# Kernel optimization log

Hardware: AMD Instinct MI355X
Metric: run time of the kernel (lower is better)

The kernel has to match this reference:

```python
import jax, jax.numpy as jnp
import numpy as np

B, Q, L, D = 4, 600, 2048, 256
H, HD, DFF, KD = 8, 32, 2048, 32  # heads, head_dim, ffn dim, gasa kernel dim
SCALE = HD ** -0.5


def setup_inputs() -> dict:
    key = jax.random.key(0)
    ks = jax.random.split(key, 24)
    w = lambda k, shape, s=0.02: (jax.random.normal(k, shape, jnp.float32) * s)
    inp = {
        "queries": jax.random.normal(ks[0], (B, Q, D), jnp.float32),
        "memory": jax.random.normal(ks[1], (B, L, D), jnp.float32),
        "memory_pos": jax.random.normal(ks[2], (B, L, 3), jnp.float32),
        "query_pos": jax.random.normal(ks[3], (B, Q, 3), jnp.float32),
        # self-attention (nn.MultiheadAttention packed in_proj)
        "sa_in_w": w(ks[4], (3 * D, D)), "sa_in_b": jnp.zeros((3 * D,), jnp.float32),
        "sa_out_w": w(ks[5], (D, D)), "sa_out_b": jnp.zeros((D,), jnp.float32),
        "norm1_g": jnp.ones((D,), jnp.float32), "norm1_b": jnp.zeros((D,), jnp.float32),
        # cross-attention projections
        "q_w": w(ks[6], (D, D)), "q_b": jnp.zeros((D,), jnp.float32),
        "k_w": w(ks[7], (D, D)), "k_b": jnp.zeros((D,), jnp.float32),
        "v_w": w(ks[8], (D, D)), "v_b": jnp.zeros((D,), jnp.float32),
        "o_w": w(ks[9], (D, D)), "o_b": jnp.zeros((D,), jnp.float32),
        "norm2_g": jnp.ones((D,), jnp.float32), "norm2_b": jnp.zeros((D,), jnp.float32),
        # GASA geometric-bias kernel: beta, MLP 1->KD->1
        "beta": jnp.asarray(1.0, jnp.float32),
        "dk_w1": w(ks[10], (KD, 1), 0.1), "dk_b1": jnp.zeros((KD,), jnp.float32),
        "dk_w2": w(ks[11], (1, KD), 0.1), "dk_b2": jnp.full((1,), -1.0, jnp.float32),
        # FFN
        "ffn_w1": w(ks[12], (DFF, D)), "ffn_b1": jnp.zeros((DFF,), jnp.float32),
        "ffn_w2": w(ks[13], (D, DFF)), "ffn_b2": jnp.zeros((D,), jnp.float32),
        "norm3_g": jnp.ones((D,), jnp.float32), "norm3_b": jnp.zeros((D,), jnp.float32),
    }
    return inp


def _ln(x, g, b, eps=1e-5):
    m = jnp.mean(x, -1, keepdims=True)
    v = jnp.mean((x - m) ** 2, -1, keepdims=True)
    return (x - m) * jax.lax.rsqrt(v + eps) * g + b


def _heads(x, wt, b):  # x:[B,N,D] -> [B,H,N,HD]
    y = x @ wt.T + b
    return y.reshape(x.shape[0], x.shape[1], H, HD).transpose(0, 2, 1, 3)


def reference(queries, memory, memory_pos, query_pos,
              sa_in_w, sa_in_b, sa_out_w, sa_out_b, norm1_g, norm1_b,
              q_w, q_b, k_w, k_b, v_w, v_b, o_w, o_b, norm2_g, norm2_b,
              beta, dk_w1, dk_b1, dk_w2, dk_b2,
              ffn_w1, ffn_b1, ffn_w2, ffn_b2, norm3_g, norm3_b):
    # ---- self-attention (post-norm, no query_pe) ----
    wq, wk, wv = jnp.split(sa_in_w, 3, axis=0)
    bq, bk, bv = jnp.split(sa_in_b, 3)
    qh = _heads(queries, wq, bq)
    kh = _heads(queries, wk, bk)
    vh = _heads(queries, wv, bv)
    a = jax.nn.softmax(jnp.einsum('bhqd,bhkd->bhqk', qh, kh) * SCALE, axis=-1)
    sa = jnp.einsum('bhqk,bhkd->bhqd', a, vh).transpose(0, 2, 1, 3).reshape(B, Q, D)
    sa = sa @ sa_out_w.T + sa_out_b
    x = _ln(queries + sa, norm1_g, norm1_b)

    # ---- GASA cross-attention ----
    Qh = _heads(x, q_w, q_b)          # [B,H,Q,HD]
    Kh = _heads(memory, k_w, k_b)     # [B,H,L,HD]
    Vh = _heads(memory, v_w, v_b)     # [B,H,L,HD]
    # cdist + learned kernel MLP, clamp to [-10, 0] (suppress-only)
    d2 = jnp.sum((query_pos[:, :, None, :] - memory_pos[:, None, :, :]) ** 2, -1)
    dist = jnp.sqrt(jnp.maximum(d2, 0.0))                     # [B,Q,L]
    hid = jax.nn.relu(dist[..., None] * dk_w1[:, 0] + dk_b1)  # [B,Q,L,KD]
    bias = (hid @ dk_w2[0]) + dk_b2[0]                        # [B,Q,L]
    bias = jnp.clip(bias, -10.0, 0.0)
    scores = jnp.einsum('bhqd,bhkd->bhqk', Qh, Kh) * SCALE + beta * bias[:, None]
    attn = jax.nn.softmax(scores, axis=-1)
    ca = jnp.einsum('bhqk,bhkd->bhqd', attn, Vh).transpose(0, 2, 1, 3).reshape(B, Q, D)
    ca = ca @ o_w.T + o_b
    x = _ln(x + ca, norm2_g, norm2_b)

    # ---- FFN (post-norm) ----
    f = jax.nn.relu(x @ ffn_w1.T + ffn_b1) @ ffn_w2.T + ffn_b2
    return _ln(x + f, norm3_g, norm3_b)
```

## Files before the change

### kernel.cpp

```cpp
#include <hip/hip_runtime.h>
#include <hip/hip_bf16.h>

typedef __hip_bfloat16 bf16;
typedef __attribute__((ext_vector_type(8))) short  short8;
typedef __attribute__((ext_vector_type(4))) short  short4v;
typedef __attribute__((ext_vector_type(4))) float  f32x4;

#define B_ 4
#define Q_ 600
#define L_ 2048
#define D_ 256
#define H_ 8
#define HD_ 32
#define DFF_ 2048
#define KD_ 32
#define SCALE_ 0.17677669529663687f
#define L2E_   1.4426950408889634f
#define SL2E_  (SCALE_ * L2E_)

template<int MODE>
__device__ __forceinline__ float ldx(const void* p, size_t i, bool f32)
{
    if (MODE == 0) return __bfloat162float(((const bf16*)p)[i]);
    if (MODE == 1) return ((const float*)p)[i];
    return f32 ? ((const float*)p)[i] : __bfloat162float(((const bf16*)p)[i]);
}
__device__ __forceinline__ short8 ld8_f32(const float* p)
{
    const float4 a = *(const float4*)p;
    const float4 b = *(const float4*)(p + 4);
    union { short8 s; bf16 h[8]; } u;
    u.h[0] = __float2bfloat16(a.x); u.h[1] = __float2bfloat16(a.y);
    u.h[2] = __float2bfloat16(a.z); u.h[3] = __float2bfloat16(a.w);
    u.h[4] = __float2bfloat16(b.x); u.h[5] = __float2bfloat16(b.y);
    u.h[6] = __float2bfloat16(b.z); u.h[7] = __float2bfloat16(b.w);
    return u.s;
}
template<int MODE>
__device__ __forceinline__ short8 ld8x(const void* p, size_t i, bool f32)
{
    if (MODE == 0) return *(const short8*)((const bf16*)p + i);
    if (MODE == 1) return ld8_f32((const float*)p + i);
    return f32 ? ld8_f32((const float*)p + i) : *(const short8*)((const bf16*)p + i);
}

__global__ __launch_bounds__(256)
void detect_kernel(const unsigned short* __restrict__ q, int* __restrict__ flag)
{
    __shared__ float red[4];
    const int tid = threadIdx.x;
    unsigned short u = q[tid];
    float f = __uint_as_float(((unsigned)(u & 0x7FFF)) << 16);
    if (f != f) f = 1e30f;
    #pragma unroll
    for (int o = 32; o > 0; o >>= 1) f = fmaxf(f, __shfl_xor(f, o));
    if ((tid & 63) == 0) red[tid >> 6] = f;
    __syncthreads();
    if (tid == 0) {
        float m = fmaxf(fmaxf(red[0], red[1]), fmaxf(red[2], red[3]));
        *flag = (m > 100.f) ? 1 : 0;
    }
}

template<int AM>
__device__ __forceinline__ void gemm_core(const void* __restrict__ A,
    const void* __restrict__ W, int M, int K, int kbeg, int kend,
    int bm, int bn, bool f32, bf16* As, bf16* Bs, f32x4 (&acc)[2][2])
{
    const int tid = threadIdx.x;
    const int w = tid >> 6, lane = tid & 63;
    const int quad = lane >> 4, l16 = lane & 15;
    const int wm = (w & 1) << 5, wn = (w >> 1) << 5;
    const int srow = tid >> 2, scol = (tid & 3) << 3;
    const int gma = (bm + srow < M) ? bm + srow : M - 1;

    short8 pa = ld8x<AM>(A, (size_t)gma * K + kbeg + scol, f32);
    short8 pb = ld8x<2>(W, (size_t)(bn + srow) * K + kbeg + scol, f32);

    for (int k0 = kbeg; k0 < kend; k0 += 32) {
        *(short8*)&As[srow * 40 + scol] = pa;
        *(short8*)&Bs[srow * 40 + scol] = pb;
        __syncthreads();
        if (k0 + 32 < kend) {
            pa = ld8x<AM>(A, (size_t)gma * K + k0 + 32 + scol, f32);
            pb = ld8x<2>(W, (size_t)(bn + srow) * K + k0 + 32 + scol, f32);
        }
        short8 af[2], bfr[2];
        #pragma unroll
        for (int t = 0; t < 2; t++) {
            af[t]  = *(const short8*)&As[(wm + t * 16 + l16) * 40 + quad * 8];
            bfr[t] = *(const short8*)&Bs[(wn + t * 16 + l16) * 40 + quad * 8];
        }
        #pragma unroll
        for (int mt = 0; mt < 2; mt++)
            #pragma unroll
            for (int nt = 0; nt < 2; nt++)
                acc[mt][nt] = __builtin_amdgcn_mfma_f32_16x16x32_bf16(
                    af[mt], bfr[nt], acc[mt][nt], 0, 0, 0);
        __syncthreads();
    }
}

template<int AM, int RM, int CM, bool RELU, int SPLIT>
__global__ __launch_bounds__(256)
void gemm_mfma(const void* __restrict__ A, const void* __restrict__ W,
               const void* __restrict__ bias, const void* __restrict__ R,
               void* __restrict__ C, int M, int N, int K,
               const int* __restrict__ flagp)
{
    const bool f32 = (*flagp != 0);
    __shared__ alignas(16) bf16 As[64 * 40];
    __shared__ alignas(16) bf16 Bs[64 * 40];
    const int bm = blockIdx.y << 6, bn = blockIdx.x << 6;
    const int KS = K / SPLIT, z = (SPLIT > 1) ? blockIdx.z : 0;

    f32x4 acc[2][2] = {{{0.f,0.f,0.f,0.f},{0.f,0.f,0.f,0.f}},
                       {{0.f,0.f,0.f,0.f},{0.f,0.f,0.f,0.f}}};
    gemm_core<AM>(A, W, M, K, z * KS, z * KS + KS, bm, bn, f32, As, Bs, acc);

    const int tid = threadIdx.x;
    const int w = tid >> 6, lane = tid & 63;
    const int quad = lane >> 4, l16 = lane & 15;
    const int wm = (w & 1) << 5, wn = (w >> 1) << 5;

    #pragma unroll
    for (int mt = 0; mt < 2; mt++) {
        #pragma unroll
        for (int r = 0; r < 4; r++) {
            const int row = bm + wm + mt * 16 + quad * 4 + r;
            if (row >= M) continue;
            #pragma unroll
            for (int nt = 0; nt < 2; nt++) {
                const int col = bn + wn + nt * 16 + l16;
                if (SPLIT > 1) {
                    ((float*)C)[((size_t)z * M + row) * N + col] = acc[mt][nt][r];
                } else {
                    float v = acc[mt][nt][r] + ldx<2>(bias, col, f32);
                    if (RM >= 0) v += ldx<RM < 0 ? 0 : RM>(R, (size_t)row * N + col, f32);
                    if (RELU) v = fmaxf(v, 0.f);
                    if (CM == 0) ((bf16*)C)[(size_t)row * N + col] = __float2bfloat16(v);
                    else         ((float*)C)[(size_t)row * N + col] = v;
                }
            }
        }
    }
}

__global__ __launch_bounds__(256)
void kv_proj(const void* __restrict__ A,
             const void* __restrict__ kw, const void* __restrict__ kb,
             const void* __restrict__ vw, const void* __restrict__ vb,
             bf16* __restrict__ kf, bf16* __restrict__ vf,
             int M, int K, const int* __restrict__ flagp)
{
    const bool f32 = (*flagp != 0);
    __shared__ alignas(16) bf16 As[64 * 40];
    __shared__ alignas(16) bf16 Bs[64 * 40];
    const int sel = blockIdx.x >> 2;
    const void* W  = sel ? vw : kw;
    const void* bs = sel ? vb : kb;
    bf16* C        = sel ? vf : kf;
    const int bn = (blockIdx.x & 3) << 6;
    const int bm = blockIdx.y << 6;

    f32x4 acc[2][2] = {{{0.f,0.f,0.f,0.f},{0.f,0.f,0.f,0.f}},
                       {{0.f,0.f,0.f,0.f},{0.f,0.f,0.f,0.f}}};
    gemm_core<2>(A, W, M, K, 0, K, bm, bn, f32, As, Bs, acc);

    const int tid = threadIdx.x;
    const int w = tid >> 6, lane = tid & 63;
    const int quad = lane >> 4, l16 = lane & 15;
    const int wm = (w & 1) << 5, wn = (w >> 1) << 5;
    #pragma unroll
    for (int mt = 0; mt < 2; mt++)
        #pragma unroll
        for (int r = 0; r < 4; r++) {
            const int row = bm + wm + mt * 16 + quad * 4 + r;
            if (row >= M) continue;
            #pragma unroll
            for (int nt = 0; nt < 2; nt++) {
                const int col = bn + wn + nt * 16 + l16;
                C[(size_t)row * 256 + col] =
                    __float2bfloat16(acc[mt][nt][r] + ldx<2>(bs, col, f32));
            }
        }
}

template<int RM, int OM, int S>
__global__ __launch_bounds__(64)
void red_ln(const float* __restrict__ P, const void* __restrict__ bias,
            const void* __restrict__ R, const void* __restrict__ gg,
            const void* __restrict__ bb, void* __restrict__ Y,
            int M, const int* __restrict__ flagp)
{
    const bool f32 = (*flagp != 0);
    const int row = blockIdx.x, lane = threadIdx.x;
    const int d0 = lane * 4;
    float v[4];
    {
        float4 a = *(const float4*)(P + ((size_t)0 * M + row) * D_ + d0);
        v[0] = a.x; v[1] = a.y; v[2] = a.z; v[3] = a.w;
    }
    #pragma unroll
    for (int s = 1; s < S; s++) {
        float4 a = *(const float4*)(P + ((size_t)s * M + row) * D_ + d0);
        v[0] += a.x; v[1] += a.y; v[2] += a.z; v[3] += a.w;
    }
    #pragma unroll
    for (int j = 0; j < 4; j++)
        v[j] += ldx<2>(bias, d0 + j, f32) + ldx<RM>(R, (size_t)row * D_ + d0 + j, f32);

    float s1 = v[0] + v[1] + v[2] + v[3];
    float s2 = v[0]*v[0] + v[1]*v[1] + v[2]*v[2] + v[3]*v[3];
    #pragma unroll
    for (int o = 32; o > 0; o >>= 1) {
        s1 += __shfl_xor(s1, o);
        s2 += __shfl_xor(s2, o);
    }
    const float mean = s1 * (1.f / D_);
    const float var = s2 * (1.f / D_) - mean * mean;
    const float rinv = rsqrtf(var + 1e-5f);
    float o[4];
    #pragma unroll
    for (int j = 0; j < 4; j++)
        o[j] = (v[j] - mean) * rinv * ldx<2>(gg, d0 + j, f32) + ldx<2>(bb, d0 + j, f32);
    const size_t i = (size_t)row * D_ + d0;
    if (OM == 1 || (OM == 2 && f32)) {
        float4 t{o[0], o[1], o[2], o[3]};
        *(float4*)((float*)Y + i) = t;
    } else {
        bf16* y = (bf16*)Y + i;
        y[0] = __float2bfloat16(o[0]); y[1] = __float2bfloat16(o[1]);
        y[2] = __float2bfloat16(o[2]); y[3] = __float2bfloat16(o[3]);
    }
}

template<bool HASBIAS, int NSEG>
__global__ __launch_bounds__(256)
void flash_attn(const bf16* __restrict__ Qm, int qs,
                const bf16* __restrict__ Km, int ks,
                const bf16* __restrict__ Vm, int vs,
                const bf16* __restrict__ biasT,
                bf16* __restrict__ pO, float* __restrict__ pml,
                int NQ, int LK)
{
    __shared__ alignas(16) bf16 Ksh[64 * 40];
    __shared__ alignas(16) bf16 Vt[48 * 72];
    __shared__ alignas(16) bf16 Psh[64 * 72];
    __shared__ alignas(16) bf16 Bsh[HASBIAS ? 64 * 72 : 8];

    const int tid = threadIdx.x;
    const int w = tid >> 6, lane = tid & 63;
    const int quad = lane >> 4, l16 = lane & 15;

    const int id = blockIdx.x;
    const int g  = ((id >> 6) << 3) + (id & 7);
    const int h  = (id >> 3) & 7;
    const int qt = g % 10;
    const int zz = g / 10;
    const int b = zz & 3, seg = zz >> 2;
    const int q0 = qt * 64;
    const int segLen = LK / NSEG;
    const int lbeg = seg * segLen, lend = lbeg + segLen;

    for (int i = tid; i < 16 * 72; i += 256) {
        int rr = 32 + i / 72, cc = i % 72;
        Vt[rr * 72 + cc] = __float2bfloat16(rr == 32 ? 1.f : 0.f);
    }

    int qrow = q0 + w * 16 + l16; if (qrow > NQ - 1) qrow = NQ - 1;
    const short8 aq = *(const short8*)(Qm + (size_t)(b * NQ + qrow) * qs + h * HD_ + quad * 8);

    f32x4 O0 = {0.f,0.f,0.f,0.f}, O1 = {0.f,0.f,0.f,0.f}, O2 = {0.f,0.f,0.f,0.f};

    const int srow = tid >> 2, sc4 = tid & 3;
    const int nch = (segLen + 63) >> 6;

    for (int ch = 0; ch < nch; ch++) {
        const int l0 = lbeg + (ch << 6);
        {
            int lg = l0 + srow; if (lg > LK - 1) lg = LK - 1;
            short8 k8 = *(const short8*)(Km + (size_t)(b * LK + lg) * ks + h * HD_ + sc4 * 8);
            *(short8*)&Ksh[srow * 40 + sc4 * 8] = k8;
            short8 v8 = *(const short8*)(Vm + (size_t)(b * LK + lg) * vs + h * HD_ + sc4 * 8);
            const int swc = srow ^ (sc4 * 16);
            #pragma unroll
            for (int j = 0; j < 8; j++)
                Vt[(sc4 * 8 + j) * 72 + swc] = ((const bf16*)&v8)[j];
            if (HASBIAS) {
                #pragma unroll
                for (int rep = 0; rep < 2; rep++) {
                    int chid = tid + rep * 256;
                    int ll = chid >> 3, qc = chid & 7;
                    int qread = q0 + qc * 8;
                    if (qread > NQ - 8) qread = NQ - 8;
                    *(short8*)&Bsh[ll * 72 + qc * 8] =
                        *(const short8*)(biasT + ((size_t)(b * LK) + l0 + ll) * Q_ + qread);
                }
            }
        }
        __syncthreads();

        f32x4 sv[4];
        #pragma unroll
        for (int jt = 0; jt < 4; jt++) {
            short8 kb = *(const short8*)&Ksh[(jt * 16 + l16) * 40 + quad * 8];
            sv[jt] = __builtin_amdgcn_mfma_f32_16x16x32_bf16(aq, kb, (f32x4){0.f,0.f,0.f,0.f}, 0, 0, 0);
        }
        if (l0 + 64 <= lend) {
            #pragma unroll
            for (int jt = 0; jt < 4; jt++) {
                if (HASBIAS) {
                    short4v bb = *(const short4v*)&Bsh[(jt * 16 + l16) * 72 + w * 16 + quad * 4];
                    #pragma unroll
                    for (int r = 0; r < 4; r++)
                        Psh[(w * 16 + quad * 4 + r) * 72 + jt * 16 + l16] =
                            __float2bfloat16(exp2f(sv[jt][r] * SL2E_ +
                                __bfloat162float(((const bf16*)&bb)[r])));
                } else {
                    #pragma unroll
                    for (int r = 0; r < 4; r++)
                        Psh[(w * 16 + quad * 4 + r) * 72 + jt * 16 + l16] =
                            __float2bfloat16(exp2f(sv[jt][r] * SL2E_));
                }
            }
        } else {
            #pragma unroll
            for (int jt = 0; jt < 4; jt++) {
                const bool valid = (l0 + jt * 16 + l16) < lend;
                #pragma unroll
                for (int r = 0; r < 4; r++)
                    Psh[(w * 16 + quad * 4 + r) * 72 + jt * 16 + l16] =
                        __float2bfloat16(valid ? exp2f(sv[jt][r] * SL2E_) : 0.f);
            }
        }
        __syncthreads();
        const int sw0 = 16 * (l16 >> 3);
        const int sw1 = 16 * (2 + (l16 >> 3));
        #pragma unroll
        for (int kt = 0; kt < 2; kt++) {
            short8 ap  = *(const short8*)&Psh[(w * 16 + l16) * 72 + kt * 32 + quad * 8];
            short8 bv0 = *(const short8*)&Vt[(l16) * 72 + ((kt * 32 + quad * 8) ^ sw0)];
            short8 bv1 = *(const short8*)&Vt[(16 + l16) * 72 + ((kt * 32 + quad * 8) ^ sw1)];
            short8 bon = *(const short8*)&Vt[(32 + l16) * 72 + kt * 32 + quad * 8];
            O0 = __builtin_amdgcn_mfma_f32_16x16x32_bf16(ap, bv0, O0, 0, 0, 0);
            O1 = __builtin_amdgcn_mfma_f32_16x16x32_bf16(ap, bv1, O1, 0, 0, 0);
            O2 = __builtin_amdgcn_mfma_f32_16x16x32_bf16(ap, bon, O2, 0, 0, 0);
        }
        __syncthreads();
    }

    #pragma unroll
    for (int r = 0; r < 4; r++) {
        const int qg = q0 + w * 16 + quad * 4 + r;
        if (qg >= NQ) continue;
        const float li = __shfl(O2[r], lane & 48);
        const float inv = 1.f / li;
        const size_t rowp = (size_t)(((seg * 4 + b) * 8) + h) * NQ + qg;
        bf16* op = pO + rowp * 32;
        op[l16]      = __float2bfloat16(O0[r] * inv);
        op[16 + l16] = __float2bfloat16(O1[r] * inv);
        if (l16 == 0) { pml[rowp * 2 + 0] = 0.f; pml[rowp * 2 + 1] = O2[r]; }
    }
}

template<int NSEG>
__global__ __launch_bounds__(256)
void attn_combine(const bf16* __restrict__ pO, const float* __restrict__ pml,
                  bf16* __restrict__ ctx, int NQ)
{
    const int t = blockIdx.x * 256 + threadIdx.x;
    const int row = t >> 5, d = t & 31;
    const int stride = 32 * NQ;
    float ms[NSEG], ls[NSEG];
    float M = -3e38f;
    #pragma unroll
    for (int s = 0; s < NSEG; s++) {
        ms[s] = pml[(size_t)(s * stride + row) * 2 + 0];
        ls[s] = pml[(size_t)(s * stride + row) * 2 + 1];
        M = fmaxf(M, ms[s]);
    }
    float W = 0.f, acc = 0.f;
    #pragma unroll
    for (int s = 0; s < NSEG; s++) {
        float wgt = ls[s] * exp2f(ms[s] - M);
        W += wgt;
        acc += wgt * __bfloat162float(pO[(size_t)(s * stride + row) * 32 + d]);
    }
    const int bh = row / NQ, q = row - bh * NQ;
    ctx[((size_t)((bh >> 3) * NQ + q)) * D_ + (bh & 7) * HD_ + d] = __float2bfloat16(acc / W);
}

__global__ __launch_bounds__(256)
void bias_pre(const void* __restrict__ qp, const void* __restrict__ mp,
              const void* __restrict__ w1, const void* __restrict__ b1,
              const void* __restrict__ w2, const void* __restrict__ b2,
              const void* __restrict__ betap, bf16* __restrict__ out,
              const int* __restrict__ flagp)
{
    const bool f32 = (*flagp != 0);
    __shared__ float sw1[KD_], sb1[KD_], sw2[KD_], scst[2];
    const int tid = threadIdx.x;
    if (tid < KD_) {
        sw1[tid] = ldx<2>(w1, tid, f32);
        sb1[tid] = ldx<2>(b1, tid, f32);
        sw2[tid] = ldx<2>(w2, tid, f32);
    }
    if (tid == 0) { scst[0] = ldx<2>(b2, 0, f32); scst[1] = L2E_ * ldx<2>(betap, 0, f32); }
    __syncthreads();
    const int idx = blockIdx.x * 256 + tid;
    const int q8 = idx % 75;
    const int t2 = idx / 75;
    const int l = t2 % L_, b = t2 / L_;
    const int q0 = q8 * 8;
    const float mx = ldx<2>(mp, (size_t)(b * L_ + l) * 3 + 0, f32);
    const float my = ldx<2>(mp, (size_t)(b * L_ + l) * 3 + 1, f32);
    const float mz = ldx<2>(mp, (size_t)(b * L_ + l) * 3 + 2, f32);
    union { short8 s; bf16 h[8]; } res;
    #pragma unroll
    for (int j = 0; j < 8; j++) {
        const int q = q0 + j;
        float dx = ldx<2>(qp, (size_t)(b * Q_ + q) * 3 + 0, f32) - mx;
        float dy = ldx<2>(qp, (size_t)(b * Q_ + q) * 3 + 1, f32) - my;
        float dz = ldx<2>(qp, (size_t)(b * Q_ + q) * 3 + 2, f32) - mz;
        float dist = sqrtf(dx * dx + dy * dy + dz * dz);
        float acc = scst[0];
        #pragma unroll
        for (int k = 0; k < KD_; k++)
            acc += fmaxf(dist * sw1[k] + sb1[k], 0.f) * sw2[k];
        acc = fminf(fmaxf(acc, -10.f), 0.f);
        res.h[j] = __float2bfloat16(scst[1] * acc);
    }
    *(short8*)(out + ((size_t)(b * L_) + l) * Q_ + q0) = res.s;
}

extern "C" void kernel_launch(void* const* d_in, const int* in_sizes, int n_in,
                              void* d_out, int out_size, void* d_ws, size_t ws_size,
                              hipStream_t stream)
{
    const void* queries   = d_in[0];
    const void* memory    = d_in[1];
    const void* memory_pos= d_in[2];
    const void* query_pos = d_in[3];
    const void* sa_in_w   = d_in[4];
    const void* sa_in_b   = d_in[5];
    const void* sa_out_w  = d_in[6];
    const void* sa_out_b  = d_in[7];
    const void* norm1_g   = d_in[8];
    const void* norm1_b   = d_in[9];
    const void* q_w  = d_in[10], *q_b  = d_in[11];
    const void* k_w  = d_in[12], *k_b  = d_in[13];
    const void* v_w  = d_in[14], *v_b  = d_in[15];
    const void* o_w  = d_in[16], *o_b  = d_in[17];
    const void* norm2_g = d_in[18], *norm2_b = d_in[19];
    const void* beta  = d_in[20];
    const void* dk_w1 = d_in[21], *dk_b1 = d_in[22];
    const void* dk_w2 = d_in[23], *dk_b2 = d_in[24];
    const void* ffn_w1 = d_in[25], *ffn_b1 = d_in[26];
    const void* ffn_w2 = d_in[27], *ffn_b2 = d_in[28];
    const void* norm3_g = d_in[29], *norm3_b = d_in[30];

    char* base = (char*)d_ws;
    bf16*  kf     = (bf16*)(base + 0);
    bf16*  vf     = (bf16*)(base + 4194304);
    float* x1     = (float*)(base + 8388608);
    bf16*  qproj  = (bf16*)(base + 10846208);
    bf16*  cactx  = (bf16*)(base + 12075008);
    float* x2     = (float*)(base + 13303808);
    bf16*  biasT  = (bf16*)(base + 15761408);
    bf16*  qkv    = (bf16*)(base + 0);
    bf16*  sactx  = (bf16*)(base + 3686400);
    bf16*  selfO  = (bf16*)(base + 4915200);
    float* selfML = (float*)(base + 7372800);
    float* P3     = (float*)(base + 15761408);
    bf16*  crossO = (bf16*)(base + 25591808);
    float* crossML= (float*)(base + 30507008);
    float* P10    = (float*)(base + 0);
    bf16*  ffnh   = (bf16*)(base + 15761408);
    float* P13    = (float*)(base + 0);
    int*   flag   = (int*)(base + 31121408);

    const dim3 blk(256);

    detect_kernel<<<1, 256, 0, stream>>>((const unsigned short*)queries, flag);
    gemm_mfma<2, -1, 0, false, 1><<<dim3(12, 38), blk, 0, stream>>>(
        queries, sa_in_w, sa_in_b, nullptr, qkv, 2400, 768, 256, flag);
    flash_attn<false, 2><<<640, blk, 0, stream>>>(
        qkv, 768, qkv + 256, 768, qkv + 512, 768, nullptr,
        selfO, selfML, 600, 600);
    attn_combine<2><<<2400, blk, 0, stream>>>(selfO, selfML, sactx, 600);
    gemm_mfma<0, -1, 1, false, 2><<<dim3(4, 38, 2), blk, 0, stream>>>(
        sactx, sa_out_w, nullptr, nullptr, P3, 2400, 256, 256, flag);
    red_ln<2, 1, 2><<<2400, 64, 0, stream>>>(
        P3, sa_out_b, queries, norm1_g, norm1_b, x1, 2400, flag);
    gemm_mfma<1, -1, 0, false, 1><<<dim3(4, 38), blk, 0, stream>>>(
        x1, q_w, q_b, nullptr, qproj, 2400, 256, 256, flag);
    kv_proj<<<dim3(8, 128), blk, 0, stream>>>(
        memory, k_w, k_b, v_w, v_b, kf, vf, 8192, 256, flag);
    bias_pre<<<2400, blk, 0, stream>>>(
        query_pos, memory_pos, dk_w1, dk_b1, dk_w2, dk_b2, beta, biasT, flag);
    flash_attn<true, 4><<<1280, blk, 0, stream>>>(
        qproj, 256, kf, 256, vf, 256, biasT,
        crossO, crossML, 600, 2048);
    attn_combine<4><<<2400, blk, 0, stream>>>(crossO, crossML, cactx, 600);
    gemm_mfma<0, -1, 1, false, 2><<<dim3(4, 38, 2), blk, 0, stream>>>(
        cactx, o_w, nullptr, nullptr, P10, 2400, 256, 256, flag);
    red_ln<1, 1, 2><<<2400, 64, 0, stream>>>(
        P10, o_b, x1, norm2_g, norm2_b, x2, 2400, flag);
    gemm_mfma<1, -1, 0, true, 1><<<dim3(32, 38), blk, 0, stream>>>(
        x2, ffn_w1, ffn_b1, nullptr, ffnh, 2400, 2048, 256, flag);
    gemm_mfma<0, -1, 1, false, 4><<<dim3(4, 38, 4), blk, 0, stream>>>(
        ffnh, ffn_w2, nullptr, nullptr, P13, 2400, 256, 2048, flag);
    red_ln<1, 2, 4><<<2400, 64, 0, stream>>>(
        P13, ffn_b2, x2, norm3_g, norm3_b, d_out, 2400, flag);
}
```

Before: 289.9 us.

## Merge input projections and bias precompute into one launch; prefetch flash-attn chunks

Combines the QKV self-attention projection, the K/V memory projection and the geometric bias precompute into a single heterogeneous kernel dispatched by block index. Independent work therefore shares one launch and fills the GPU concurrently, and the workspace layout is reassigned so these buffers do not alias. The flash attention loop now loads the next chunk's K, V and bias into registers while computing on the current one, and drops one barrier per chunk. This removes launch gaps and hides global load latency, but it raises register pressure and relies on the remaining barrier to keep the shared-memory reuse safe.

```diff
diff --git a/kernel.cpp b/kernel.cpp
--- a/kernel.cpp
+++ b/kernel.cpp
@@ -98,6 +98,95 @@
                 acc[mt][nt] = __builtin_amdgcn_mfma_f32_16x16x32_bf16(
                     af[mt], bfr[nt], acc[mt][nt], 0, 0, 0);
         __syncthreads();
+    }
+}
+
+__device__ __forceinline__ void gemm64_bf16out(const void* A, const void* W,
+    const void* bs, bf16* C, int M, int N, int K, int bm, int bn, bool f32,
+    bf16* As, bf16* Bs)
+{
+    f32x4 acc[2][2] = {{{0.f,0.f,0.f,0.f},{0.f,0.f,0.f,0.f}},
+                       {{0.f,0.f,0.f,0.f},{0.f,0.f,0.f,0.f}}};
+    gemm_core<2>(A, W, M, K, 0, K, bm, bn, f32, As, Bs, acc);
+    const int tid = threadIdx.x;
+    const int w = tid >> 6, lane = tid & 63;
+    const int quad = lane >> 4, l16 = lane & 15;
+    const int wm = (w & 1) << 5, wn = (w >> 1) << 5;
+    #pragma unroll
+    for (int mt = 0; mt < 2; mt++)
+        #pragma unroll
+        for (int r = 0; r < 4; r++) {
+            const int row = bm + wm + mt * 16 + quad * 4 + r;
+            if (row >= M) continue;
+            #pragma unroll
+            for (int nt = 0; nt < 2; nt++) {
+                const int col = bn + wn + nt * 16 + l16;
+                C[(size_t)row * N + col] =
+                    __float2bfloat16(acc[mt][nt][r] + ldx<2>(bs, col, f32));
+            }
+        }
+}
+
+__global__ __launch_bounds__(256)
+void input_stage(const void* __restrict__ queries, const void* __restrict__ sa_in_w,
+                 const void* __restrict__ sa_in_b, bf16* __restrict__ qkv,
+                 const void* __restrict__ memory,
+                 const void* __restrict__ kw, const void* __restrict__ kb,
+                 const void* __restrict__ vw, const void* __restrict__ vb,
+                 bf16* __restrict__ kf, bf16* __restrict__ vf,
+                 const void* __restrict__ qp, const void* __restrict__ mp,
+                 const void* __restrict__ w1, const void* __restrict__ b1,
+                 const void* __restrict__ w2, const void* __restrict__ b2,
+                 const void* __restrict__ betap, bf16* __restrict__ biasT,
+                 const int* __restrict__ flagp)
+{
+    const bool f32 = (*flagp != 0);
+    __shared__ alignas(16) bf16 sAB[2 * 64 * 40];
+    const int id = blockIdx.x;
+    if (id < 456) {
+        gemm64_bf16out(queries, sa_in_w, sa_in_b, qkv, 2400, 768, 256,
+                       (id / 12) << 6, (id % 12) << 6, f32, sAB, sAB + 64 * 40);
+    } else if (id < 1480) {
+        const int t = id - 456;
+        const int bx = t & 7, sel = bx >> 2;
+        gemm64_bf16out(memory, sel ? vw : kw, sel ? vb : kb, sel ? vf : kf,
+                       8192, 256, 256, (t >> 3) << 6, (bx & 3) << 6, f32,
+                       sAB, sAB + 64 * 40);
+    } else {
+        float* fs = (float*)sAB;
+        float *sw1 = fs, *sb1 = fs + 32, *sw2 = fs + 64, *scst = fs + 96;
+        const int tid = threadIdx.x;
+        if (tid < KD_) {
+            sw1[tid] = ldx<2>(w1, tid, f32);
+            sb1[tid] = ldx<2>(b1, tid, f32);
+            sw2[tid] = ldx<2>(w2, tid, f32);
+        }
+        if (tid == 0) { scst[0] = ldx<2>(b2, 0, f32); scst[1] = L2E_ * ldx<2>(betap, 0, f32); }
+        __syncthreads();
+        const int idx = (id - 1480) * 256 + tid;
+        const int q8 = idx % 75;
+        const int t2 = idx / 75;
+        const int l = t2 % L_, b = t2 / L_;
+        const int q0 = q8 * 8;
+        const float mx = ldx<2>(mp, (size_t)(b * L_ + l) * 3 + 0, f32);
+        const float my = ldx<2>(mp, (size_t)(b * L_ + l) * 3 + 1, f32);
+        const float mz = ldx<2>(mp, (size_t)(b * L_ + l) * 3 + 2, f32);
+        union { short8 s; bf16 h[8]; } res;
+        #pragma unroll
+        for (int j = 0; j < 8; j++) {
+            const int q = q0 + j;
+            float dx = ldx<2>(qp, (size_t)(b * Q_ + q) * 3 + 0, f32) - mx;
+            float dy = ldx<2>(qp, (size_t)(b * Q_ + q) * 3 + 1, f32) - my;
+            float dz = ldx<2>(qp, (size_t)(b * Q_ + q) * 3 + 2, f32) - mz;
+            float dist = sqrtf(dx * dx + dy * dy + dz * dz);
+            float acc = scst[0];
+            #pragma unroll
+            for (int k = 0; k < KD_; k++)
+                acc += fmaxf(dist * sw1[k] + sb1[k], 0.f) * sw2[k];
+            acc = fminf(fmaxf(acc, -10.f), 0.f);
+            res.h[j] = __float2bfloat16(scst[1] * acc);
+        }
+        *(short8*)(biasT + ((size_t)(b * L_) + l) * Q_ + q0) = res.s;
     }
 }
 
@@ -146,46 +235,6 @@
     }
 }
 
-__global__ __launch_bounds__(256)
-void kv_proj(const void* __restrict__ A,
-             const void* __restrict__ kw, const void* __restrict__ kb,
-             const void* __restrict__ vw, const void* __restrict__ vb,
-             bf16* __restrict__ kf, bf16* __restrict__ vf,
-             int M, int K, const int* __restrict__ flagp)
-{
-    const bool f32 = (*flagp != 0);
-    __shared__ alignas(16) bf16 As[64 * 40];
-    __shared__ alignas(16) bf16 Bs[64 * 40];
-    const int sel = blockIdx.x >> 2;
-    const void* W  = sel ? vw : kw;
-    const void* bs = sel ? vb : kb;
-    bf16* C        = sel ? vf : kf;
-    const int bn = (blockIdx.x & 3) << 6;
-    const int bm = blockIdx.y << 6;
-
-    f32x4 acc[2][2] = {{{0.f,0.f,0.f,0.f},{0.f,0.f,0.f,0.f}},
-                       {{0.f,0.f,0.f,0.f},{0.f,0.f,0.f,0.f}}};
-    gemm_core<2>(A, W, M, K, 0, K, bm, bn, f32, As, Bs, acc);
-
-    const int tid = threadIdx.x;
-    const int w = tid >> 6, lane = tid & 63;
-    const int quad = lane >> 4, l16 = lane & 15;
-    const int wm = (w & 1) << 5, wn = (w >> 1) << 5;
-    #pragma unroll
-    for (int mt = 0; mt < 2; mt++)
-        #pragma unroll
-        for (int r = 0; r < 4; r++) {
-            const int row = bm + wm + mt * 16 + quad * 4 + r;
-            if (row >= M) continue;
-            #pragma unroll
-            for (int nt = 0; nt < 2; nt++) {
-                const int col = bn + wn + nt * 16 + l16;
-                C[(size_t)row * 256 + col] =
-                    __float2bfloat16(acc[mt][nt][r] + ldx<2>(bs, col, f32));
-            }
-        }
-}
-
 template<int RM, int OM, int S>
 __global__ __launch_bounds__(64)
 void red_ln(const float* __restrict__ P, const void* __restrict__ bias,
@@ -276,30 +325,43 @@
     const int srow = tid >> 2, sc4 = tid & 3;
     const int nch = (segLen + 63) >> 6;
 
+    short8 k8, v8, bb8[2];
+    auto load_chunk = [&](int l0c) {
+        int lg = l0c + srow; if (lg > LK - 1) lg = LK - 1;
+        k8 = *(const short8*)(Km + (size_t)(b * LK + lg) * ks + h * HD_ + sc4 * 8);
+        v8 = *(const short8*)(Vm + (size_t)(b * LK + lg) * vs + h * HD_ + sc4 * 8);
+        if (HASBIAS) {
+            #pragma unroll
+            for (int rep = 0; rep < 2; rep++) {
+                int chid = tid + rep * 256;
+                int ll = chid >> 3, qc = chid & 7;
+                int qread = q0 + qc * 8;
+                if (qread > NQ - 8) qread = NQ - 8;
+                bb8[rep] = *(const short8*)(biasT + ((size_t)(b * LK) + l0c + ll) * Q_ + qread);
+            }
+        }
+    };
+    load_chunk(lbeg);
+
     for (int ch = 0; ch < nch; ch++) {
         const int l0 = lbeg + (ch << 6);
+        *(short8*)&Ksh[srow * 40 + sc4 * 8] = k8;
         {
-            int lg = l0 + srow; if (lg > LK - 1) lg = LK - 1;
-            short8 k8 = *(const short8*)(Km + (size_t)(b * LK + lg) * ks + h * HD_ + sc4 * 8);
-            *(short8*)&Ksh[srow * 40 + sc4 * 8] = k8;
-            short8 v8 = *(const short8*)(Vm + (size_t)(b * LK + lg) * vs + h * HD_ + sc4 * 8);
             const int swc = srow ^ (sc4 * 16);
             #pragma unroll
             for (int j = 0; j < 8; j++)
                 Vt[(sc4 * 8 + j) * 72 + swc] = ((const bf16*)&v8)[j];
-            if (HASBIAS) {
-                #pragma unroll
-                for (int rep = 0; rep < 2; rep++) {
-                    int chid = tid + rep * 256;
-                    int ll = chid >> 3, qc = chid & 7;
-                    int qread = q0 + qc * 8;
-                    if (qread > NQ - 8) qread = NQ - 8;
-                    *(short8*)&Bsh[ll * 72 + qc * 8] =
-                        *(const short8*)(biasT + ((size_t)(b * LK) + l0 + ll) * Q_ + qread);
-                }
+        }
+        if (HASBIAS) {
+            #pragma unroll
+            for (int rep = 0; rep < 2; rep++) {
+                int chid = tid + rep * 256;
+                int ll = chid >> 3, qc = chid & 7;
+                *(short8*)&Bsh[ll * 72 + qc * 8] = bb8[rep];
             }
         }
         __syncthreads();
+        if (ch + 1 < nch) load_chunk(l0 + 64);
 
         f32x4 sv[4];
         #pragma unroll
@@ -334,7 +396,6 @@
                         __float2bfloat16(valid ? exp2f(sv[jt][r] * SL2E_) : 0.f);
             }
         }
-        __syncthreads();
         const int sw0 = 16 * (l16 >> 3);
         const int sw1 = 16 * (2 + (l16 >> 3));
         #pragma unroll
@@ -389,49 +450,6 @@
     }
     const int bh = row / NQ, q = row - bh * NQ;
     ctx[((size_t)((bh >> 3) * NQ + q)) * D_ + (bh & 7) * HD_ + d] = __float2bfloat16(acc / W);
-}
-
-__global__ __launch_bounds__(256)
-void bias_pre(const void* __restrict__ qp, const void* __restrict__ mp,
-              const void* __restrict__ w1, const void* __restrict__ b1,
-              const void* __restrict__ w2, const void* __restrict__ b2,
-              const void* __restrict__ betap, bf16* __restrict__ out,
-              const int* __restrict__ flagp)
-{
-    const bool f32 = (*flagp != 0);
-    __shared__ float sw1[KD_], sb1[KD_], sw2[KD_], scst[2];
-    const int tid = threadIdx.x;
-    if (tid < KD_) {
-        sw1[tid] = ldx<2>(w1, tid, f32);
-        sb1[tid] = ldx<2>(b1, tid, f32);
-        sw2[tid] = ldx<2>(w2, tid, f32);
-    }
-    if (tid == 0) { scst[0] = ldx<2>(b2, 0, f32); scst[1] = L2E_ * ldx<2>(betap, 0, f32); }
-    __syncthreads();
-    const int idx = blockIdx.x * 256 + tid;
-    const int q8 = idx % 75;
-    const int t2 = idx / 75;
-    const int l = t2 % L_, b = t2 / L_;
-    const int q0 = q8 * 8;
-    const float mx = ldx<2>(mp, (size_t)(b * L_ + l) * 3 + 0, f32);
-    const float my = ldx<2>(mp, (size_t)(b * L_ + l) * 3 + 1, f32);
-    const float mz = ldx<2>(mp, (size_t)(b * L_ + l) * 3 + 2, f32);
-    union { short8 s; bf16 h[8]; } res;
-    #pragma unroll
-    for (int j = 0; j < 8; j++) {
-        const int q = q0 + j;
-        float dx = ldx<2>(qp, (size_t)(b * Q_ + q) * 3 + 0, f32) - mx;
-        float dy = ldx<2>(qp, (size_t)(b * Q_ + q) * 3 + 1, f32) - my;
-        float dz = ldx<2>(qp, (size_t)(b * Q_ + q) * 3 + 2, f32) - mz;
-        float dist = sqrtf(dx * dx + dy * dy + dz * dz);
-        float acc = scst[0];
-        #pragma unroll
-        for (int k = 0; k < KD_; k++)
-            acc += fmaxf(dist * sw1[k] + sb1[k], 0.f) * sw2[k];
-        acc = fminf(fmaxf(acc, -10.f), 0.f);
-        res.h[j] = __float2bfloat16(scst[1] * acc);
-    }
-    *(short8*)(out + ((size_t)(b * L_) + l) * Q_ + q0) = res.s;
 }
 
 extern "C" void kernel_launch(void* const* d_in, const int* in_sizes, int n_in,
@@ -463,28 +481,30 @@
     char* base = (char*)d_ws;
     bf16*  kf     = (bf16*)(base + 0);
     bf16*  vf     = (bf16*)(base + 4194304);
-    float* x1     = (float*)(base + 8388608);
-    bf16*  qproj  = (bf16*)(base + 10846208);
-    bf16*  cactx  = (bf16*)(base + 12075008);
-    float* x2     = (float*)(base + 13303808);
-    bf16*  biasT  = (bf16*)(base + 15761408);
-    bf16*  qkv    = (bf16*)(base + 0);
-    bf16*  sactx  = (bf16*)(base + 3686400);
-    bf16*  selfO  = (bf16*)(base + 4915200);
-    float* selfML = (float*)(base + 7372800);
-    float* P3     = (float*)(base + 15761408);
-    bf16*  crossO = (bf16*)(base + 25591808);
-    float* crossML= (float*)(base + 30507008);
+    bf16*  biasT  = (bf16*)(base + 8388608);
+    bf16*  qkv    = (bf16*)(base + 18219008);
+    bf16*  sactx  = (bf16*)(base + 18219008);
+    bf16*  selfO  = (bf16*)(base + 21905408);
+    float* selfML = (float*)(base + 24363008);
+    float* P3     = (float*)(base + 21905408);
+    float* x1     = (float*)(base + 26820608);
+    bf16*  qproj  = (bf16*)(base + 29278208);
+    bf16*  crossO = (bf16*)(base + 21905408);
+    float* crossML= (float*)(base + 19447808);
+    bf16*  cactx  = (bf16*)(base + 18219008);
     float* P10    = (float*)(base + 0);
-    bf16*  ffnh   = (bf16*)(base + 15761408);
-    float* P13    = (float*)(base + 0);
-    int*   flag   = (int*)(base + 31121408);
+    float* x2     = (float*)(base + 4915200);
+    bf16*  ffnh   = (bf16*)(base + 8388608);
+    float* P13    = (float*)(base + 18219008);
+    int*   flag   = (int*)(base + 30507008);
 
     const dim3 blk(256);
 
     detect_kernel<<<1, 256, 0, stream>>>((const unsigned short*)queries, flag);
-    gemm_mfma<2, -1, 0, false, 1><<<dim3(12, 38), blk, 0, stream>>>(
-        queries, sa_in_w, sa_in_b, nullptr, qkv, 2400, 768, 256, flag);
+    input_stage<<<3880, blk, 0, stream>>>(
+        queries, sa_in_w, sa_in_b, qkv,
+        memory, k_w, k_b, v_w, v_b, kf, vf,
+        query_pos, memory_pos, dk_w1, dk_b1, dk_w2, dk_b2, beta, biasT, flag);
     flash_attn<false, 2><<<640, blk, 0, stream>>>(
         qkv, 768, qkv + 256, 768, qkv + 512, 768, nullptr,
         selfO, selfML, 600, 600);
@@ -495,10 +515,6 @@
         P3, sa_out_b, queries, norm1_g, norm1_b, x1, 2400, flag);
     gemm_mfma<1, -1, 0, false, 1><<<dim3(4, 38), blk, 0, stream>>>(
         x1, q_w, q_b, nullptr, qproj, 2400, 256, 256, flag);
-    kv_proj<<<dim3(8, 128), blk, 0, stream>>>(
-        memory, k_w, k_b, v_w, v_b, kf, vf, 8192, 256, flag);
-    bias_pre<<<2400, blk, 0, stream>>>(
-        query_pos, memory_pos, dk_w1, dk_b1, dk_w2, dk_b2, beta, biasT, flag);
     flash_attn<true, 4><<<1280, blk, 0, stream>>>(
         qproj, 256, kf, 256, vf, 256, biasT,
         crossO, crossML, 600, 2048);
```

Result: slower. 496.8 us (+71.4%).
